# Performance work log

Measured on AMD Instinct MI355X. Metric: run time of the kernel, lower is better.

The kernel has to match this reference:

```python
import jax, jax.numpy as jnp
import numpy as np

B, KVH, HPK, D = 4, 8, 4, 128          # batch, n_kv_heads, n_heads_per_kv, head_size
SEQ_KV = 4096                           # cached history length
SEQ = SEQ_KV + 1                        # history + current token
K, LOCAL_K, SINK, RANK = 512, 128, 4, 32


def gather(t, axis, i):
    """Broadcasting take_along_axis, mirroring the torch `gather` helper."""
    axis = axis % t.ndim
    tgt = list(t.shape)
    tgt[axis] = i.shape[axis]
    return jnp.take_along_axis(t, jnp.broadcast_to(i, tgt), axis)


def sparse_q_score(q, key_cpu_t, cur_key_t):
    # q: (B,KVH,HPK,1,D); key_cpu_t: (B,KVH,D,SEQ_KV); cur_key_t: (B,KVH,1,D,1)
    absq = jnp.abs(q).sum(2, keepdims=True)                    # (B,KVH,1,1,D)
    _, idx = jax.lax.top_k(absq, RANK)                         # (B,KVH,1,1,RANK)
    q_proj = gather(q, -1, idx)                                # (B,KVH,HPK,1,RANK)
    idx_t = jnp.swapaxes(idx, -1, -2)                          # (B,KVH,1,RANK,1)
    k_hist = gather(key_cpu_t[:, :, None], -2, idx_t)          # (B,KVH,1,RANK,SEQ_KV)
    k_cur = gather(cur_key_t, -2, idx_t)                       # (B,KVH,1,RANK,1)
    k_proj = jnp.concatenate([k_hist, k_cur], -1)              # (B,KVH,1,RANK,SEQ)
    scale = jnp.sqrt(jnp.abs(q_proj).sum(-1) / jnp.abs(q).sum(-1) * D)[..., None]
    return jnp.matmul(q_proj, k_proj) / scale                  # (B,KVH,HPK,1,SEQ)


def setup_inputs():
    key = jax.random.key(0)
    ks = jax.random.split(key, 6)
    query = jax.random.normal(ks[0], (B, KVH * HPK, 1, D), jnp.float32)
    k = jax.random.normal(ks[1], (B, KVH, 1, D), jnp.float32)
    v = jax.random.normal(ks[2], (B, KVH, 1, D), jnp.float32)
    logmask = jnp.zeros((B, KVH * HPK, 1, SEQ), jnp.float32)
    key_cpu = jax.random.normal(ks[3], (B, KVH, SEQ_KV, D), jnp.float32)
    value_cpu = jax.random.normal(ks[4], (B, KVH, SEQ_KV, D), jnp.float32)
    s_key_cpu = jnp.swapaxes(key_cpu, -1, -2)                  # head-size-contiguous copy
    mean_v = jax.random.normal(ks[5], (B, KVH, 1, 1, D), jnp.float32)
    return {"query": query, "key": k, "value": v, "logmask": logmask,
            "key_cpu": key_cpu, "value_cpu": value_cpu,
            "s_key_cpu": s_key_cpu, "mean_v": mean_v}


def reference(query, key, value, logmask, key_cpu, value_cpu, s_key_cpu, mean_v):
    q = query.reshape(B, KVH, HPK, 1, D)
    k = key.reshape(B, KVH, 1, 1, D)
    v = value.reshape(B, KVH, 1, 1, D)
    lm = logmask.reshape(B, KVH, HPK, 1, SEQ)
    # approximate scores over the full key history + current key
    score = (sparse_q_score(q, s_key_cpu, jnp.swapaxes(k, 3, 4)) + lm).astype(jnp.float32)
    # causal index over history (excluding current token): 0 = most recent unmasked
    neg = jnp.isneginf(lm[..., :-1])
    ci = jnp.where(neg, -1,
                   jnp.cumsum((~neg)[..., ::-1].astype(jnp.int32), -1)[..., ::-1] - 1)
    is_local = (0 <= ci) & (ci < LOCAL_K)
    is_sink = ci >= SEQ - SINK - 1
    fmax = jnp.finfo(jnp.float32).max
    topk_score = jnp.where(is_local | is_sink, fmax, score[..., :-1]).sum(2, keepdims=True)
    kk = min(K + SINK, SEQ)
    _, indices = jax.lax.top_k(topk_score, kk)                 # (B,KVH,1,1,kk)
    # running mean value update
    mean_v_new = (mean_v * (SEQ - 1) + v.astype(jnp.float32)) / SEQ
    # weight reallocation to the mean value
    norm = jax.nn.softmax(score, -1)
    kv_weight = gather(norm, -1, indices).sum(-1) + norm[..., -1]  # (B,KVH,HPK,1)
    # gather selected K/V and append current token
    kv_idx = indices[..., 0, :, None]                          # (B,KVH,1,kk,1)
    key_g = jnp.concatenate([gather(key_cpu[:, :, None], -2, kv_idx), k], -2)   # (B,KVH,1,kk+1,D)
    val_g = jnp.concatenate([gather(value_cpu[:, :, None], -2, kv_idx), v], -2)
    cur_idx = jnp.full(indices.shape[:-1] + (1,), SEQ - 1, indices.dtype)
    lm_g = gather(lm, -1, jnp.concatenate([indices, cur_idx], -1))  # (B,KVH,HPK,1,kk+1)
    # dense attention over the reduced key set
    scores = jnp.matmul(q, jnp.swapaxes(key_g, -1, -2)) * (D ** -0.5) + lm_g
    weights = jax.nn.softmax(scores.astype(jnp.float32), -1) * kv_weight[..., None]
    out = jnp.matmul(weights, val_g) + (1.0 - kv_weight[..., None]) * mean_v_new
    return out.reshape(B, KVH * HPK, 1, D), weights.reshape(B, KVH * HPK, 1, kk + 1)
```

## Files before the change

kernel.cpp:

```cpp
#include <hip/hip_runtime.h>
#include <math.h>

#define NBH 32
#define HPKN 4
#define DN 128
#define SEQKV 4096
#define SEQN 4097
#define SSTR 4100
#define RANKN 32
#define KSEL 516
#define SINKN 4
#define LOCALK 128
#define NMASK 132
#define NTOP 384
#define NCHUNK 16

__global__ __launch_bounds__(256) void k2_scores(
    const float* __restrict__ q, const float* __restrict__ key,
    const float* __restrict__ skey, const float* __restrict__ lm,
    float* __restrict__ scores, float* __restrict__ tk,
    float2* __restrict__ partials) {
  int bh = blockIdx.y;
  int s0 = blockIdx.x << 8;
  int t = threadIdx.x;
  int wave = t >> 6, lane = t & 63;
  __shared__ float qv[4][128];
  __shared__ float absq[128];
  __shared__ int sel[RANKN];
  __shared__ float qp[4][RANKN];
  __shared__ float wred[4][4];

  {
    float v0 = q[(size_t)bh * 512 + t];
    float v1 = q[(size_t)bh * 512 + 256 + t];
    qv[t >> 7][t & 127] = v0;
    qv[2 + (t >> 7)][t & 127] = v1;
  }
  __syncthreads();
  if (t < 128)
    absq[t] = fabsf(qv[0][t]) + fabsf(qv[1][t]) + fabsf(qv[2][t]) + fabsf(qv[3][t]);
  __syncthreads();
  if (t < 128) {
    float a = absq[t];
    int rank = 0;
    for (int e = 0; e < 128; ++e) {
      float ae = absq[e];
      rank += (ae > a) || (ae == a && e < t);
    }
    if (rank < RANKN) sel[rank] = t;
  }
  __syncthreads();
  {
    float fa = fabsf(qv[wave][lane]) + fabsf(qv[wave][lane + 64]);
    for (int off = 32; off > 0; off >>= 1) fa += __shfl_down(fa, off);
    float full = __shfl(fa, 0);
    float qsel = (lane < RANKN) ? qv[wave][sel[lane]] : 0.f;
    float sv = fabsf(qsel);
    for (int off = 32; off > 0; off >>= 1) sv += __shfl_down(sv, off);
    float selsum = __shfl(sv, 0);
    float scale = sqrtf(selsum / full * 128.f);
    if (lane < RANKN) qp[wave][lane] = qsel / scale;
  }
  __syncthreads();

  if (blockIdx.x == 0) {
    float kv = (lane < RANKN) ? key[bh * 128 + sel[lane]] : 0.f;
    float pr = (lane < RANKN) ? qp[wave][lane] * kv : 0.f;
    for (int off = 32; off > 0; off >>= 1) pr += __shfl_down(pr, off);
    if (lane == 0)
      scores[(size_t)(bh * 4 + wave) * SSTR + SEQKV] =
          pr + lm[(size_t)(bh * 4 + wave) * SEQN + SEQKV];
  }

  const float* kb = skey + (size_t)bh * 128 * 4096;
  float a0 = 0, a1 = 0, a2 = 0, a3 = 0;
#pragma unroll 8
  for (int r = 0; r < RANKN; ++r) {
    float k0 = kb[((size_t)sel[r] << 12) + s0 + t];
    a0 += qp[0][r] * k0;
    a1 += qp[1][r] * k0;
    a2 += qp[2][r] * k0;
    a3 += qp[3][r] * k0;
  }
  float sc[4];
  {
    int s = s0 + t;
    sc[0] = a0 + lm[(size_t)(bh * 4 + 0) * SEQN + s];
    sc[1] = a1 + lm[(size_t)(bh * 4 + 1) * SEQN + s];
    sc[2] = a2 + lm[(size_t)(bh * 4 + 2) * SEQN + s];
    sc[3] = a3 + lm[(size_t)(bh * 4 + 3) * SEQN + s];
    float sum = sc[0] + sc[1] + sc[2] + sc[3];
#pragma unroll
    for (int p = 0; p < 4; ++p)
      scores[(size_t)(bh * 4 + p) * SSTR + s] = sc[p];
    tk[(bh << 12) + s] = sum;
  }

#pragma unroll
  for (int p = 0; p < 4; ++p) {
    float mx = sc[p];
    for (int off = 32; off > 0; off >>= 1) mx = fmaxf(mx, __shfl_down(mx, off));
    if (lane == 0) wred[wave][p] = mx;
  }
  __syncthreads();
  float bm[4];
#pragma unroll
  for (int p = 0; p < 4; ++p)
    bm[p] = fmaxf(fmaxf(wred[0][p], wred[1][p]), fmaxf(wred[2][p], wred[3][p]));
  __syncthreads();
#pragma unroll
  for (int p = 0; p < 4; ++p) {
    float e = expf(sc[p] - bm[p]);
    for (int off = 32; off > 0; off >>= 1) e += __shfl_down(e, off);
    if (lane == 0) wred[wave][p] = e;
  }
  __syncthreads();
  if (t < 4) {
    float s = wred[0][t] + wred[1][t] + wred[2][t] + wred[3][t];
    partials[(size_t)(bh * 4 + t) * NCHUNK + blockIdx.x] = make_float2(bm[t], s);
  }
}

__global__ __launch_bounds__(256) void k3_topk(
    const float* __restrict__ tk, int* __restrict__ indices) {
  int bh = blockIdx.x;
  int t = threadIdx.x;
  int lane = t & 63;
  __shared__ unsigned us[4096];
  __shared__ unsigned hist[2048];
  __shared__ unsigned long long binlist[2048];
  __shared__ unsigned long long selk[512];
  __shared__ unsigned chunkSum[32];
  __shared__ int c1, c2, binB_s, nAbove_s, needed_s;

  {
    const float4* tk4 = (const float4*)(tk + (bh << 12));
    for (int i = t; i < 1024; i += 256) {
      float4 v = tk4[i];
      unsigned b0 = __float_as_uint(v.x), b1 = __float_as_uint(v.y);
      unsigned b2 = __float_as_uint(v.z), b3 = __float_as_uint(v.w);
      us[i * 4 + 0] = (b0 & 0x80000000u) ? ~b0 : (b0 | 0x80000000u);
      us[i * 4 + 1] = (b1 & 0x80000000u) ? ~b1 : (b1 | 0x80000000u);
      us[i * 4 + 2] = (b2 & 0x80000000u) ? ~b2 : (b2 | 0x80000000u);
      us[i * 4 + 3] = (b3 & 0x80000000u) ? ~b3 : (b3 | 0x80000000u);
    }
  }
  for (int i = t; i < 2048; i += 256) hist[i] = 0;
  if (t == 0) { c1 = 0; c2 = 0; }
  __syncthreads();

  for (int s = SINKN + t; s < SEQKV - LOCALK; s += 256)
    atomicAdd(&hist[us[s] >> 21], 1u);
  __syncthreads();

  if (t < 32) {
    unsigned sum = 0;
    for (int i = 0; i < 64; ++i) sum += hist[t * 64 + i];
    chunkSum[t] = sum;
  }
  __syncthreads();

  if (t < 64) {
    int l = t;
    unsigned x = (l < 32) ? chunkSum[l] : 0;
    unsigned sfx = x;
    for (int off = 1; off < 64; off <<= 1) {
      unsigned y = __shfl_down(sfx, off);
      if (l + off < 64) sfx += y;
    }
    unsigned above = sfx - x;
    bool hit = (l < 32) && (above < NTOP) && (above + x >= NTOP);
    unsigned long long mask = __ballot(hit);
    int C = __ffsll(mask) - 1;
    unsigned aboveC = __shfl(above, C);
    unsigned h = hist[C * 64 + l];
    unsigned sfx2 = h;
    for (int off = 1; off < 64; off <<= 1) {
      unsigned y = __shfl_down(sfx2, off);
      if (l + off < 64) sfx2 += y;
    }
    unsigned above2 = aboveC + (sfx2 - h);
    bool hit2 = (above2 < NTOP) && (above2 + h >= NTOP);
    unsigned long long mask2 = __ballot(hit2);
    int lB = __ffsll(mask2) - 1;
    if (l == lB) {
      binB_s = C * 64 + l;
      nAbove_s = (int)above2;
      needed_s = NTOP - (int)above2;
    }
  }
  __syncthreads();
  unsigned B = (unsigned)binB_s;
  int nAbove = nAbove_s, needed = needed_s;

  for (int s0 = SINKN; s0 < SEQKV - LOCALK; s0 += 256) {
    int s = s0 + t;
    bool valid = (s < SEQKV - LOCALK);
    unsigned u = valid ? us[s] : 0u;
    unsigned bin = u >> 21;
    bool win = valid && (bin > B);
    bool bnd = valid && (bin == B);
    unsigned long long mw = __ballot(win);
    unsigned long long mb = __ballot(bnd);
    int bw = 0, bb = 0;
    if (lane == 0) {
      if (mw) bw = atomicAdd(&c1, __popcll(mw));
      if (mb) bb = atomicAdd(&c2, __popcll(mb));
    }
    bw = __shfl(bw, 0);
    bb = __shfl(bb, 0);
    unsigned long long lmask = (1ULL << lane) - 1ULL;
    unsigned long long key = ((unsigned long long)u << 32) | (unsigned)(~s);
    if (win) selk[bw + __popcll(mw & lmask)] = key;
    if (bnd) {
      int pos = bb + __popcll(mb & lmask);
      if (pos < 2048) binlist[pos] = key;
    }
  }
  __syncthreads();
  int m2 = c2;
  int p2 = 1;
  while (p2 < m2) p2 <<= 1;
  for (int i = m2 + t; i < p2; i += 256) binlist[i] = 0ULL;
  __syncthreads();
  for (int k = 2; k <= p2; k <<= 1)
    for (int j = k >> 1; j > 0; j >>= 1) {
      for (int i = t; i < p2; i += 256) {
        int ixj = i ^ j;
        if (ixj > i) {
          bool desc = ((i & k) == 0);
          unsigned long long a = binlist[i], bb2 = binlist[ixj];
          if ((a < bb2) == desc) { binlist[i] = bb2; binlist[ixj] = a; }
        }
      }
      __syncthreads();
    }
  for (int i = t; i < needed; i += 256) selk[nAbove + i] = binlist[i];
  for (int i = NTOP + t; i < 512; i += 256) selk[i] = 0ULL;
  __syncthreads();

  unsigned long long e0 = selk[t], e1 = selk[t + 256];
  int i1 = t + 256;
  for (int k = 2; k <= 512; k <<= 1) {
    for (int j = k >> 1; j > 0; j >>= 1) {
      if (j == 256) {
        if (e0 < e1) { unsigned long long tmp = e0; e0 = e1; e1 = tmp; }
      } else if (j >= 64) {
        selk[t] = e0; selk[i1] = e1;
        __syncthreads();
        unsigned long long p0 = selk[t ^ j], p1 = selk[i1 ^ j];
        __syncthreads();
        bool d0 = ((t & k) == 0), l0 = ((t & j) == 0);
        e0 = (d0 == l0) ? (e0 > p0 ? e0 : p0) : (e0 < p0 ? e0 : p0);
        bool d1 = ((i1 & k) == 0), l1 = ((i1 & j) == 0);
        e1 = (d1 == l1) ? (e1 > p1 ? e1 : p1) : (e1 < p1 ? e1 : p1);
      } else {
        unsigned long long p0 = __shfl_xor(e0, j);
        unsigned long long p1 = __shfl_xor(e1, j);
        bool d0 = ((t & k) == 0), l0 = ((t & j) == 0);
        e0 = (d0 == l0) ? (e0 > p0 ? e0 : p0) : (e0 < p0 ? e0 : p0);
        bool d1 = ((i1 & k) == 0);
        e1 = (d1 == l0) ? (e1 > p1 ? e1 : p1) : (e1 < p1 ? e1 : p1);
      }
    }
  }

  if (t < SINKN) indices[bh * KSEL + t] = t;
  for (int i = t; i < LOCALK; i += 256)
    indices[bh * KSEL + SINKN + i] = (SEQKV - LOCALK) + i;
  indices[bh * KSEL + NMASK + t] = (int)(~(unsigned)(e0 & 0xFFFFFFFFu));
  if (t < NTOP - 256)
    indices[bh * KSEL + NMASK + 256 + t] = (int)(~(unsigned)(e1 & 0xFFFFFFFFu));
}

__global__ __launch_bounds__(256) void k5_qk(
    const float* __restrict__ q, const float* __restrict__ key,
    const float* __restrict__ lm, const float* __restrict__ key_cpu,
    const int* __restrict__ indices, float* __restrict__ s2_g) {
  int bh = blockIdx.y;
  int t = threadIdx.x;
  int wave = t >> 6, lane = t & 63;
  __shared__ float qs[512];
  __shared__ int sidx[KSEL];
  qs[t] = q[((size_t)bh * 4 << 7) + t];
  qs[t + 256] = q[((size_t)bh * 4 << 7) + t + 256];
  for (int j = t; j < KSEL; j += 256) sidx[j] = indices[bh * KSEL + j];
  __syncthreads();

  const float rsqd = 0.08838834764831845f;
  float q0a = qs[lane * 2], q0b = qs[lane * 2 + 1];
  float q1a = qs[128 + lane * 2], q1b = qs[128 + lane * 2 + 1];
  float q2a = qs[256 + lane * 2], q2b = qs[256 + lane * 2 + 1];
  float q3a = qs[384 + lane * 2], q3b = qs[384 + lane * 2 + 1];

  int jv[5], sjv[5];
  float2 kk[5];
#pragma unroll
  for (int i = 0; i < 5; ++i) {
    int j = (blockIdx.x << 2) + wave + 104 * i;
    jv[i] = j;
    int sj = SEQKV;
    const float* krow = key + ((size_t)bh << 7);
    if (j < KSEL) {
      sj = sidx[j];
      krow = key_cpu + ((((size_t)bh << 12) + sj) << 7);
    }
    sjv[i] = sj;
    kk[i] = ((const float2*)krow)[lane];
  }

#pragma unroll
  for (int i = 0; i < 5; ++i) {
    int j = jv[i];
    if (j > KSEL) continue;
    float2 kv = kk[i];
    float p0 = q0a * kv.x + q0b * kv.y;
    float p1 = q1a * kv.x + q1b * kv.y;
    float p2 = q2a * kv.x + q2b * kv.y;
    float p3 = q3a * kv.x + q3b * kv.y;
    for (int off = 32; off > 0; off >>= 1) {
      p0 += __shfl_down(p0, off);
      p1 += __shfl_down(p1, off);
      p2 += __shfl_down(p2, off);
      p3 += __shfl_down(p3, off);
    }
    if (lane == 0) {
      size_t lmb = (size_t)bh * 4 * SEQN + sjv[i];
      s2_g[(bh * 4 + 0) * 520 + j] = p0 * rsqd + lm[lmb + 0 * SEQN];
      s2_g[(bh * 4 + 1) * 520 + j] = p1 * rsqd + lm[lmb + 1 * SEQN];
      s2_g[(bh * 4 + 2) * 520 + j] = p2 * rsqd + lm[lmb + 2 * SEQN];
      s2_g[(bh * 4 + 3) * 520 + j] = p3 * rsqd + lm[lmb + 3 * SEQN];
    }
  }
}

__global__ __launch_bounds__(256) void k6_stats(
    const float* __restrict__ scores, const float2* __restrict__ partials,
    const int* __restrict__ indices, const float* __restrict__ s2_g,
    const float* __restrict__ value, const float* __restrict__ mean_v,
    float* __restrict__ out_w, float* __restrict__ w_g,
    float* __restrict__ out) {
  int bhp = blockIdx.x;
  int bh = bhp >> 2;
  int t = threadIdx.x;
  __shared__ int sidx[KSEL];
  __shared__ float red[256];
  __shared__ float bc;

  for (int j = t; j < KSEL; j += 256) sidx[j] = indices[bh * KSEL + j];
  __syncthreads();

  const float* srow = scores + (size_t)bhp * SSTR;
  float cur = srow[SEQKV];

  float m = cur, sumexp;
  {
    float2 pc[NCHUNK];
#pragma unroll
    for (int c = 0; c < NCHUNK; ++c) {
      pc[c] = partials[(size_t)bhp * NCHUNK + c];
      m = fmaxf(m, pc[c].x);
    }
    float s = expf(cur - m);
#pragma unroll
    for (int c = 0; c < NCHUNK; ++c) s += pc[c].y * expf(pc[c].x - m);
    sumexp = s;
  }

  float ss = 0.f;
  for (int j = t; j < KSEL; j += 256) ss += expf(srow[sidx[j]] - m);
  red[t] = ss; __syncthreads();
  for (int st = 128; st > 0; st >>= 1) {
    if (t < st) red[t] += red[t + st];
    __syncthreads();
  }
  float kvw;
  if (t == 0) bc = (red[0] + expf(cur - m)) / sumexp;
  __syncthreads();
  kvw = bc; __syncthreads();

  const float* s2r = s2_g + (size_t)bhp * 520;
  float mx2 = -INFINITY;
  for (int j = t; j < KSEL + 1; j += 256) mx2 = fmaxf(mx2, s2r[j]);
  red[t] = mx2; __syncthreads();
  for (int st = 128; st > 0; st >>= 1) {
    if (t < st) red[t] = fmaxf(red[t], red[t + st]);
    __syncthreads();
  }
  float m2 = red[0]; __syncthreads();
  float se2 = 0.f;
  for (int j = t; j < KSEL + 1; j += 256) se2 += expf(s2r[j] - m2);
  red[t] = se2; __syncthreads();
  for (int st = 128; st > 0; st >>= 1) {
    if (t < st) red[t] += red[t + st];
    __syncthreads();
  }
  float inv = kvw / red[0];

  for (int j = t; j < KSEL + 1; j += 256) {
    float w = expf(s2r[j] - m2) * inv;
    out_w[(size_t)bhp * (KSEL + 1) + j] = w;
    w_g[(size_t)bhp * 520 + j] = w;
  }

  if (t < 128) {
    float vcur = value[((size_t)bh << 7) + t];
    float mvn = (mean_v[((size_t)bh << 7) + t] * 4096.f + vcur) / 4097.f;
    out[((size_t)bhp << 7) + t] = (1.f - kvw) * mvn;
  }
}

__global__ __launch_bounds__(256) void k7_wv(
    const float* __restrict__ value, const float* __restrict__ value_cpu,
    const int* __restrict__ indices, const float* __restrict__ w_g,
    float* __restrict__ out) {
  int bh = blockIdx.y;
  int c0 = blockIdx.x << 5;
  int t = threadIdx.x;
  int d = t & 127, half = t >> 7;
  __shared__ int sidx[32];
  __shared__ float wsh[4][32];
  __shared__ float red[2][4][128];

  int nj = min(32, KSEL + 1 - c0);
  if (t < nj) {
    int j = c0 + t;
    sidx[t] = (j < KSEL) ? indices[bh * KSEL + j] : -1;
  }
  if (t < 128) {
    int p = t >> 5, jl = t & 31;
    wsh[p][jl] = (jl < nj) ? w_g[(size_t)(bh * 4 + p) * 520 + c0 + jl] : 0.f;
  }
  __syncthreads();

  const float* vbase = value_cpu + ((size_t)bh << 19);
  const float* vcurrow = value + ((size_t)bh << 7);
  float a0 = 0, a1 = 0, a2 = 0, a3 = 0;
  int jl = half;
  for (; jl + 6 < nj; jl += 8) {
    int s0 = sidx[jl], s1 = sidx[jl + 2], s2i = sidx[jl + 4], s3 = sidx[jl + 6];
    const float* r0 = (s0 >= 0) ? vbase + ((size_t)s0 << 7) : vcurrow;
    const float* r1 = (s1 >= 0) ? vbase + ((size_t)s1 << 7) : vcurrow;
    const float* r2 = (s2i >= 0) ? vbase + ((size_t)s2i << 7) : vcurrow;
    const float* r3 = (s3 >= 0) ? vbase + ((size_t)s3 << 7) : vcurrow;
    float v0 = r0[d], v1 = r1[d], v2 = r2[d], v3 = r3[d];
    a0 += wsh[0][jl] * v0; a1 += wsh[1][jl] * v0;
    a2 += wsh[2][jl] * v0; a3 += wsh[3][jl] * v0;
    a0 += wsh[0][jl + 2] * v1; a1 += wsh[1][jl + 2] * v1;
    a2 += wsh[2][jl + 2] * v1; a3 += wsh[3][jl + 2] * v1;
    a0 += wsh[0][jl + 4] * v2; a1 += wsh[1][jl + 4] * v2;
    a2 += wsh[2][jl + 4] * v2; a3 += wsh[3][jl + 4] * v2;
    a0 += wsh[0][jl + 6] * v3; a1 += wsh[1][jl + 6] * v3;
    a2 += wsh[2][jl + 6] * v3; a3 += wsh[3][jl + 6] * v3;
  }
  for (; jl < nj; jl += 2) {
    int sj = sidx[jl];
    const float* vrow = (sj >= 0) ? vbase + ((size_t)sj << 7) : vcurrow;
    float v = vrow[d];
    a0 += wsh[0][jl] * v;
    a1 += wsh[1][jl] * v;
    a2 += wsh[2][jl] * v;
    a3 += wsh[3][jl] * v;
  }
  red[half][0][d] = a0; red[half][1][d] = a1;
  red[half][2][d] = a2; red[half][3][d] = a3;
  __syncthreads();
  if (half == 0) {
#pragma unroll
    for (int p = 0; p < 4; ++p) {
      float s = red[0][p][d] + red[1][p][d];
      atomicAdd(&out[(size_t)(bh * 4 + p) * 128 + d], s);
    }
  }
}

extern "C" void kernel_launch(void* const* d_in, const int* in_sizes, int n_in,
                              void* d_out, int out_size, void* d_ws, size_t ws_size,
                              hipStream_t stream) {
  const float* query     = (const float*)d_in[0];
  const float* key       = (const float*)d_in[1];
  const float* value     = (const float*)d_in[2];
  const float* logmask   = (const float*)d_in[3];
  const float* key_cpu   = (const float*)d_in[4];
  const float* value_cpu = (const float*)d_in[5];
  const float* s_key_cpu = (const float*)d_in[6];
  const float* mean_v    = (const float*)d_in[7];

  float* out   = (float*)d_out;
  float* out_w = out + 16384;

  char* ws = (char*)d_ws;
  int*    indices  = (int*)(ws + 20480);
  float*  scores   = (float*)(ws + 86528);
  float*  tk       = (float*)(ws + 2185728);
  float*  s2_g     = (float*)(ws + 2710016);
  float*  w_g      = (float*)(ws + 2976256);
  float2* partials = (float2*)(ws + 3242496);

  hipLaunchKernelGGL(k2_scores, dim3(NCHUNK, NBH), dim3(256), 0, stream,
                     query, key, s_key_cpu, logmask, scores, tk, partials);
  hipLaunchKernelGGL(k3_topk, dim3(NBH), dim3(256), 0, stream,
                     tk, indices);
  hipLaunchKernelGGL(k5_qk, dim3(26, NBH), dim3(256), 0, stream,
                     query, key, logmask, key_cpu, indices, s2_g);
  hipLaunchKernelGGL(k6_stats, dim3(128), dim3(256), 0, stream,
                     scores, partials, indices, s2_g, value, mean_v,
                     out_w, w_g, out);
  hipLaunchKernelGGL(k7_wv, dim3(17, NBH), dim3(256), 0, stream,
                     value, value_cpu, indices, w_g, out);
}
```

Measured before the change: 223.8 us.

## Fuse softmax stats kernel into weighted-value kernel and zero output in topk

```diff
diff --git a/kernel.cpp b/kernel.cpp
--- a/kernel.cpp
+++ b/kernel.cpp
@@ -122,7 +122,8 @@
 }
 
 __global__ __launch_bounds__(256) void k3_topk(
-    const float* __restrict__ tk, int* __restrict__ indices) {
+    const float* __restrict__ tk, int* __restrict__ indices,
+    float* __restrict__ out) {
   int bh = blockIdx.x;
   int t = threadIdx.x;
   int lane = t & 63;
@@ -132,6 +133,8 @@
   __shared__ unsigned long long selk[512];
   __shared__ unsigned chunkSum[32];
   __shared__ int c1, c2, binB_s, nAbove_s, needed_s;
+
+  for (int i = t; i < 512; i += 256) out[(size_t)bh * 512 + i] = 0.f;
 
   {
     const float4* tk4 = (const float4*)(tk + (bh << 12));
@@ -334,102 +337,75 @@
   }
 }
 
-__global__ __launch_bounds__(256) void k6_stats(
-    const float* __restrict__ scores, const float2* __restrict__ partials,
-    const int* __restrict__ indices, const float* __restrict__ s2_g,
-    const float* __restrict__ value, const float* __restrict__ mean_v,
-    float* __restrict__ out_w, float* __restrict__ w_g,
-    float* __restrict__ out) {
-  int bhp = blockIdx.x;
-  int bh = bhp >> 2;
-  int t = threadIdx.x;
-  __shared__ int sidx[KSEL];
-  __shared__ float red[256];
-  __shared__ float bc;
-
-  for (int j = t; j < KSEL; j += 256) sidx[j] = indices[bh * KSEL + j];
-  __syncthreads();
-
-  const float* srow = scores + (size_t)bhp * SSTR;
-  float cur = srow[SEQKV];
-
-  float m = cur, sumexp;
-  {
-    float2 pc[NCHUNK];
-#pragma unroll
-    for (int c = 0; c < NCHUNK; ++c) {
-      pc[c] = partials[(size_t)bhp * NCHUNK + c];
-      m = fmaxf(m, pc[c].x);
-    }
-    float s = expf(cur - m);
-#pragma unroll
-    for (int c = 0; c < NCHUNK; ++c) s += pc[c].y * expf(pc[c].x - m);
-    sumexp = s;
-  }
-
-  float ss = 0.f;
-  for (int j = t; j < KSEL; j += 256) ss += expf(srow[sidx[j]] - m);
-  red[t] = ss; __syncthreads();
-  for (int st = 128; st > 0; st >>= 1) {
-    if (t < st) red[t] += red[t + st];
-    __syncthreads();
-  }
-  float kvw;
-  if (t == 0) bc = (red[0] + expf(cur - m)) / sumexp;
-  __syncthreads();
-  kvw = bc; __syncthreads();
-
-  const float* s2r = s2_g + (size_t)bhp * 520;
-  float mx2 = -INFINITY;
-  for (int j = t; j < KSEL + 1; j += 256) mx2 = fmaxf(mx2, s2r[j]);
-  red[t] = mx2; __syncthreads();
-  for (int st = 128; st > 0; st >>= 1) {
-    if (t < st) red[t] = fmaxf(red[t], red[t + st]);
-    __syncthreads();
-  }
-  float m2 = red[0]; __syncthreads();
-  float se2 = 0.f;
-  for (int j = t; j < KSEL + 1; j += 256) se2 += expf(s2r[j] - m2);
-  red[t] = se2; __syncthreads();
-  for (int st = 128; st > 0; st >>= 1) {
-    if (t < st) red[t] += red[t + st];
-    __syncthreads();
-  }
-  float inv = kvw / red[0];
-
-  for (int j = t; j < KSEL + 1; j += 256) {
-    float w = expf(s2r[j] - m2) * inv;
-    out_w[(size_t)bhp * (KSEL + 1) + j] = w;
-    w_g[(size_t)bhp * 520 + j] = w;
-  }
-
-  if (t < 128) {
-    float vcur = value[((size_t)bh << 7) + t];
-    float mvn = (mean_v[((size_t)bh << 7) + t] * 4096.f + vcur) / 4097.f;
-    out[((size_t)bhp << 7) + t] = (1.f - kvw) * mvn;
-  }
-}
-
 __global__ __launch_bounds__(256) void k7_wv(
     const float* __restrict__ value, const float* __restrict__ value_cpu,
-    const int* __restrict__ indices, const float* __restrict__ w_g,
-    float* __restrict__ out) {
+    const float* __restrict__ mean_v, const float* __restrict__ scores,
+    const float2* __restrict__ partials, const int* __restrict__ indices,
+    const float* __restrict__ s2_g, float* __restrict__ out,
+    float* __restrict__ out_w) {
   int bh = blockIdx.y;
   int c0 = blockIdx.x << 5;
   int t = threadIdx.x;
+  int wave = t >> 6, lane = t & 63;
   int d = t & 127, half = t >> 7;
-  __shared__ int sidx[32];
+
+  __shared__ int sidx[KSEL];
+  __shared__ float s2s[4][520];
+  __shared__ float kvws[4], m2s[4], invs[4];
   __shared__ float wsh[4][32];
-  __shared__ float red[2][4][128];
-
-  int nj = min(32, KSEL + 1 - c0);
-  if (t < nj) {
-    int j = c0 + t;
-    sidx[t] = (j < KSEL) ? indices[bh * KSEL + j] : -1;
-  }
+  __shared__ float vred[2][4][128];
+
+  for (int j = t; j < KSEL; j += 256) sidx[j] = indices[bh * KSEL + j];
+#pragma unroll
+  for (int p = 0; p < 4; ++p)
+    for (int j = t; j < KSEL + 1; j += 256)
+      s2s[p][j] = s2_g[(size_t)(bh * 4 + p) * 520 + j];
+  __syncthreads();
+
+  {
+    const int p = wave;
+    const int bhp = bh * 4 + p;
+    const float* srow = scores + (size_t)bhp * SSTR;
+    float cur = srow[SEQKV];
+    float2 pc = (lane < NCHUNK) ? partials[(size_t)bhp * NCHUNK + lane]
+                                : make_float2(-INFINITY, 0.f);
+    float mA = fmaxf(pc.x, cur);
+    for (int off = 32; off > 0; off >>= 1) mA = fmaxf(mA, __shfl_down(mA, off));
+    mA = __shfl(mA, 0);
+    float sA = (lane < NCHUNK) ? pc.y * expf(pc.x - mA) : 0.f;
+    for (int off = 32; off > 0; off >>= 1) sA += __shfl_down(sA, off);
+    sA = __shfl(sA, 0) + expf(cur - mA);
+    float selm = 0.f;
+    for (int j = lane; j < KSEL; j += 64) selm += expf(srow[sidx[j]] - mA);
+    for (int off = 32; off > 0; off >>= 1) selm += __shfl_down(selm, off);
+    selm = __shfl(selm, 0);
+    float kvw = (selm + expf(cur - mA)) / sA;
+
+    float mx2 = -INFINITY;
+    for (int j = lane; j < KSEL + 1; j += 64) mx2 = fmaxf(mx2, s2s[p][j]);
+    for (int off = 32; off > 0; off >>= 1) mx2 = fmaxf(mx2, __shfl_down(mx2, off));
+    mx2 = __shfl(mx2, 0);
+    float se2 = 0.f;
+    for (int j = lane; j < KSEL + 1; j += 64) se2 += expf(s2s[p][j] - mx2);
+    for (int off = 32; off > 0; off >>= 1) se2 += __shfl_down(se2, off);
+    se2 = __shfl(se2, 0);
+    if (lane == 0) {
+      kvws[p] = kvw;
+      m2s[p] = mx2;
+      invs[p] = kvw / se2;
+    }
+  }
+  __syncthreads();
+
+  const int nj = min(32, KSEL + 1 - c0);
   if (t < 128) {
     int p = t >> 5, jl = t & 31;
-    wsh[p][jl] = (jl < nj) ? w_g[(size_t)(bh * 4 + p) * 520 + c0 + jl] : 0.f;
+    float w = 0.f;
+    if (jl < nj) {
+      w = expf(s2s[p][c0 + jl] - m2s[p]) * invs[p];
+      out_w[(size_t)(bh * 4 + p) * (KSEL + 1) + c0 + jl] = w;
+    }
+    wsh[p][jl] = w;
   }
   __syncthreads();
 
@@ -438,7 +414,11 @@
   float a0 = 0, a1 = 0, a2 = 0, a3 = 0;
   int jl = half;
   for (; jl + 6 < nj; jl += 8) {
-    int s0 = sidx[jl], s1 = sidx[jl + 2], s2i = sidx[jl + 4], s3 = sidx[jl + 6];
+    int j0 = c0 + jl, j1 = c0 + jl + 2, j2 = c0 + jl + 4, j3 = c0 + jl + 6;
+    int s0 = (j0 < KSEL) ? sidx[j0] : -1;
+    int s1 = (j1 < KSEL) ? sidx[j1] : -1;
+    int s2i = (j2 < KSEL) ? sidx[j2] : -1;
+    int s3 = (j3 < KSEL) ? sidx[j3] : -1;
     const float* r0 = (s0 >= 0) ? vbase + ((size_t)s0 << 7) : vcurrow;
     const float* r1 = (s1 >= 0) ? vbase + ((size_t)s1 << 7) : vcurrow;
     const float* r2 = (s2i >= 0) ? vbase + ((size_t)s2i << 7) : vcurrow;
@@ -454,7 +434,8 @@
     a2 += wsh[2][jl + 6] * v3; a3 += wsh[3][jl + 6] * v3;
   }
   for (; jl < nj; jl += 2) {
-    int sj = sidx[jl];
+    int jj = c0 + jl;
+    int sj = (jj < KSEL) ? sidx[jj] : -1;
     const float* vrow = (sj >= 0) ? vbase + ((size_t)sj << 7) : vcurrow;
     float v = vrow[d];
     a0 += wsh[0][jl] * v;
@@ -462,13 +443,16 @@
     a2 += wsh[2][jl] * v;
     a3 += wsh[3][jl] * v;
   }
-  red[half][0][d] = a0; red[half][1][d] = a1;
-  red[half][2][d] = a2; red[half][3][d] = a3;
+  vred[half][0][d] = a0; vred[half][1][d] = a1;
+  vred[half][2][d] = a2; vred[half][3][d] = a3;
   __syncthreads();
   if (half == 0) {
+    float vcur = value[((size_t)bh << 7) + d];
+    float mvn = (mean_v[((size_t)bh << 7) + d] * 4096.f + vcur) / 4097.f;
 #pragma unroll
     for (int p = 0; p < 4; ++p) {
-      float s = red[0][p][d] + red[1][p][d];
+      float s = vred[0][p][d] + vred[1][p][d];
+      if (blockIdx.x == 16) s += (1.f - kvws[p]) * mvn;
       atomicAdd(&out[(size_t)(bh * 4 + p) * 128 + d], s);
     }
   }
@@ -494,18 +478,15 @@
   float*  scores   = (float*)(ws + 86528);
   float*  tk       = (float*)(ws + 2185728);
   float*  s2_g     = (float*)(ws + 2710016);
-  float*  w_g      = (float*)(ws + 2976256);
   float2* partials = (float2*)(ws + 3242496);
 
   hipLaunchKernelGGL(k2_scores, dim3(NCHUNK, NBH), dim3(256), 0, stream,
                      query, key, s_key_cpu, logmask, scores, tk, partials);
   hipLaunchKernelGGL(k3_topk, dim3(NBH), dim3(256), 0, stream,
-                     tk, indices);
+                     tk, indices, out);
   hipLaunchKernelGGL(k5_qk, dim3(26, NBH), dim3(256), 0, stream,
                      query, key, logmask, key_cpu, indices, s2_g);
-  hipLaunchKernelGGL(k6_stats, dim3(128), dim3(256), 0, stream,
-                     scores, partials, indices, s2_g, value, mean_v,
-                     out_w, w_g, out);
   hipLaunchKernelGGL(k7_wv, dim3(17, NBH), dim3(256), 0, stream,
-                     value, value_cpu, indices, w_g, out);
+                     value, value_cpu, mean_v, scores, partials, indices,
+                     s2_g, out, out_w);
 }
```

New measurement: 227.9 us. No clear change (+1.8%).
